# Kernel tuning notes

Measured on AMD Instinct MI355X. Metric: run time of the kernel, lower is better.

Reference implementation:

```python
import jax, jax.numpy as jnp
import numpy as np

B, C, W, H = 8, 256, 64, 64
DQK = C // 8  # 32


def setup_inputs() -> dict:
    key = jax.random.key(0)
    ks = jax.random.split(key, 5)
    x = jax.random.normal(ks[0], (B, C, W, H), dtype=jnp.float32)
    # 1x1 conv weights as [out_ch, in_ch]; scaled ~ spectral-normalized magnitude
    w_q = jax.random.normal(ks[1], (DQK, C), dtype=jnp.float32) * (1.0 / np.sqrt(C))
    w_k = jax.random.normal(ks[2], (DQK, C), dtype=jnp.float32) * (1.0 / np.sqrt(C))
    w_v = jax.random.normal(ks[3], (C, C), dtype=jnp.float32) * (1.0 / np.sqrt(C))
    b_q = jnp.zeros((DQK,), dtype=jnp.float32)
    b_k = jnp.zeros((DQK,), dtype=jnp.float32)
    b_v = jnp.zeros((C,), dtype=jnp.float32)
    gamma = jax.random.normal(ks[4], (1,), dtype=jnp.float32)
    return {"x": x, "w_q": w_q, "b_q": b_q, "w_k": w_k, "b_k": b_k,
            "w_v": w_v, "b_v": b_v, "gamma": gamma}


def reference(x, w_q, b_q, w_k, b_k, w_v, b_v, gamma):
    b, c, w, h = x.shape
    n = w * h
    xf = x.reshape(b, c, n)  # [B, C, N]
    # 1x1 convs == channel-mixing matmuls
    q = jnp.einsum('dc,bcn->bnd', w_q, xf) + b_q  # [B, N, Dqk]
    k = jnp.einsum('dc,bcn->bdn', w_k, xf) + b_k[None, :, None]  # [B, Dqk, N]
    v = jnp.einsum('oc,bcn->bon', w_v, xf) + b_v[None, :, None]  # [B, C, N]
    energy = jnp.einsum('bnd,bdm->bnm', q, k)  # [B, N, N]
    attn = jax.nn.softmax(energy, axis=-1)
    # out[b,c,i] = sum_j v[b,c,j] * attn[b,i,j]  (bmm(v, attn^T))
    out = jnp.einsum('bcj,bij->bci', v, attn).reshape(b, c, w, h)
    return gamma[0] * out + x
```

## Files before the change

kernel.cpp:

```cpp
#include <hip/hip_runtime.h>
#include <hip/hip_bf16.h>

typedef __attribute__((ext_vector_type(8))) short short8;
typedef __attribute__((ext_vector_type(4))) float f32x4;
typedef __attribute__((ext_vector_type(16))) float f32x16;

#define NB 8
#define NC 256
#define NN 4096
#define ND 32
#define NCH 16
#define LOG2E 1.44269504088896340736f

#define PIDX(row, col) (((row) << 8) + ((col) ^ (((row) & 15) << 3)))

static __device__ __forceinline__ ushort f2bf(float f) {
  __hip_bfloat16 h = __float2bfloat16(f);
  return reinterpret_cast<ushort&>(h);
}

__global__ __launch_bounds__(256, 4)
void proj_kernel(const float* __restrict__ x,
                 const float* __restrict__ wq, const float* __restrict__ bq,
                 const float* __restrict__ wk, const float* __restrict__ bk,
                 const float* __restrict__ wv, const float* __restrict__ bv,
                 ushort* __restrict__ qk, ushort* __restrict__ vt) {
  __shared__ float Xs[16][128];
  __shared__ float Ws[16][64];
  const int n0 = blockIdx.x * 128;
  const int o0 = blockIdx.y * 64;
  const int b  = blockIdx.z;
  const int t  = threadIdx.x;
  const int og4 = t & 15;
  const int ng  = t >> 4;

  float acc[4][8];
#pragma unroll
  for (int i = 0; i < 4; ++i)
#pragma unroll
    for (int j = 0; j < 8; ++j) acc[i][j] = 0.f;

  const int xs_r = t >> 4;
  const int xs_c = (t & 15) * 4;
  const int ws_o = t & 63;
  const int ws_c = (t >> 6) * 4;
  const float* wrow;
  {
    const int o = o0 + ws_o;
    if (o < 32)      wrow = wq + (size_t)o * NC;
    else if (o < 64) wrow = wk + (size_t)(o - 32) * NC;
    else             wrow = wv + (size_t)(o - 64) * NC;
  }

  for (int c0 = 0; c0 < NC; c0 += 16) {
    __syncthreads();
    const float* xsrc = x + ((size_t)(b * NC + c0 + xs_r)) * NN + n0;
    *(float4*)&Xs[xs_r][xs_c]      = *(const float4*)(xsrc + xs_c);
    *(float4*)&Xs[xs_r][64 + xs_c] = *(const float4*)(xsrc + 64 + xs_c);
    {
      const float4 wv4 = *(const float4*)(wrow + c0 + ws_c);
      Ws[ws_c + 0][ws_o] = wv4.x;
      Ws[ws_c + 1][ws_o] = wv4.y;
      Ws[ws_c + 2][ws_o] = wv4.z;
      Ws[ws_c + 3][ws_o] = wv4.w;
    }
    __syncthreads();
#pragma unroll
    for (int cc = 0; cc < 16; ++cc) {
      const float4 wv4 = *(const float4*)&Ws[cc][og4 * 4];
      const float4 xa  = *(const float4*)&Xs[cc][ng * 8];
      const float4 xb  = *(const float4*)&Xs[cc][ng * 8 + 4];
      const float wvv[4] = {wv4.x, wv4.y, wv4.z, wv4.w};
      const float xaa[8] = {xa.x, xa.y, xa.z, xa.w, xb.x, xb.y, xb.z, xb.w};
#pragma unroll
      for (int i = 0; i < 4; ++i)
#pragma unroll
        for (int j = 0; j < 8; ++j) acc[i][j] += wvv[i] * xaa[j];
    }
  }

  if (blockIdx.y == 0) {
    float bb[4], sc[4];
#pragma unroll
    for (int i = 0; i < 4; ++i) {
      const int o = og4 * 4 + i;
      bb[i] = (o < 32) ? bq[o] : bk[o - 32];
      sc[i] = (o < 32) ? LOG2E : 1.0f;
    }
#pragma unroll
    for (int j = 0; j < 8; ++j) {
      union { ushort u[4]; uint2 v; } pk;
#pragma unroll
      for (int i = 0; i < 4; ++i) pk.u[i] = f2bf((acc[i][j] + bb[i]) * sc[i]);
      *(uint2*)(qk + ((size_t)(b * NN + n0 + ng * 8 + j)) * 64 + og4 * 4) = pk.v;
    }
  } else {
#pragma unroll
    for (int i = 0; i < 4; ++i) {
      const int c = o0 - 64 + og4 * 4 + i;
      const float bb = bv[c];
      union { ushort u[8]; uint4 v; } pk;
#pragma unroll
      for (int j = 0; j < 8; ++j) pk.u[j] = f2bf(acc[i][j] + bb);
      *(uint4*)(vt + ((size_t)(b * NC + c)) * NN + n0 + ng * 8) = pk.v;
    }
  }
}

__global__ __launch_bounds__(512, 1)
void attn_kernel(const ushort* __restrict__ qk, const ushort* __restrict__ vt,
                 const float* __restrict__ x, const float* __restrict__ gamma,
                 float* __restrict__ out) {
  __shared__ __align__(16) ushort P[2][128 * 256];
  __shared__ __align__(16) float lL[128];

  const int lin  = blockIdx.x;
  const int b    = lin & 7;
  const int i0   = (lin >> 3) * 128;
  const int t    = threadIdx.x;
  const int w    = t >> 6;
  const int lane = t & 63;
  const int g16  = lane >> 4;
  const int c16  = lane & 15;
  const int l5   = lane >> 5;
  const int c32  = lane & 31;

  const f32x4 zero = {0.f, 0.f, 0.f, 0.f};
  const bool isS = (w < 4);

  const int prow0 = w * 32 + c16;
  const int prow1 = prow0 + 16;
  short8 qf0, qf1;
  short8 kf[8];
  float lp0 = 0.f, lp1 = 0.f;
  const ushort* kbase = qk + ((size_t)b * NN) * 64 + 32 + g16 * 8;
  if (isS) {
    qf0 = *(const short8*)(qk + ((size_t)(b * NN + i0 + prow0)) * 64 + g16 * 8);
    qf1 = *(const short8*)(qk + ((size_t)(b * NN + i0 + prow1)) * 64 + g16 * 8);
  }

  const int p = w - 4;
  f32x16 OA[4], OB[4];
  const ushort* vbA = nullptr; const ushort* vbB = nullptr;
  if (!isS) {
#pragma unroll
    for (int isub = 0; isub < 4; ++isub)
#pragma unroll
      for (int e = 0; e < 16; ++e) { OA[isub][e] = 0.f; OB[isub][e] = 0.f; }
    vbA = vt + ((size_t)(b * NC + p * 64 + c32)) * NN + l5 * 8;
    vbB = vt + ((size_t)(b * NC + p * 64 + 32 + c32)) * NN + l5 * 8;
  }

  for (int iv = 0; iv <= NCH; ++iv) {
    if (isS) {
      if (iv < NCH) {
        ushort* Pb = P[iv & 1];
        const ushort* kch = kbase + (size_t)iv * 256 * 64;
#pragma unroll
        for (int h = 0; h < 2; ++h) {
#pragma unroll
          for (int jt = 0; jt < 8; ++jt)
            kf[jt] = *(const short8*)(
                kch + (size_t)(h * 128 + jt * 16 + c16) * 64);
#pragma unroll
          for (int jt = 0; jt < 8; ++jt) {
            const f32x4 s0 = __builtin_amdgcn_mfma_f32_16x16x32_bf16(
                kf[jt], qf0, zero, 0, 0, 0);
            const f32x4 s1 = __builtin_amdgcn_mfma_f32_16x16x32_bf16(
                kf[jt], qf1, zero, 0, 0, 0);
            union { ushort u[4]; uint2 v; } pk0, pk1;
#pragma unroll
            for (int r = 0; r < 4; ++r) {
              const float e0 = exp2f(s0[r]);
              const float e1 = exp2f(s1[r]);
              lp0 += e0; lp1 += e1;
              pk0.u[r] = f2bf(e0); pk1.u[r] = f2bf(e1);
            }
            const int col = h * 128 + jt * 16 + g16 * 4;
            *(uint2*)&Pb[PIDX(prow0, col)] = pk0.v;
            *(uint2*)&Pb[PIDX(prow1, col)] = pk1.v;
          }
        }
      } else {
        lp0 += __shfl_xor(lp0, 16); lp0 += __shfl_xor(lp0, 32);
        lp1 += __shfl_xor(lp1, 16); lp1 += __shfl_xor(lp1, 32);
        if (g16 == 0) { lL[prow0] = lp0; lL[prow1] = lp1; }
      }
    } else if (iv >= 1) {
      const int ch = iv - 1;
      const ushort* Pb = P[ch & 1];
      const int j0 = ch * 256;
      __builtin_amdgcn_s_setprio(1);
#pragma unroll
      for (int ji = 0; ji < 16; ++ji) {
        const int jo = ji * 16;
        const short8 vf0 = *(const short8*)(vbA + j0 + jo);
        const short8 vf1 = *(const short8*)(vbB + j0 + jo);
#pragma unroll
        for (int isub = 0; isub < 4; ++isub) {
          const short8 pa =
              *(const short8*)&Pb[PIDX(isub * 32 + c32, jo + l5 * 8)];
          OA[isub] = __builtin_amdgcn_mfma_f32_32x32x16_bf16(
              pa, vf0, OA[isub], 0, 0, 0);
          OB[isub] = __builtin_amdgcn_mfma_f32_32x32x16_bf16(
              pa, vf1, OB[isub], 0, 0, 0);
        }
      }
      __builtin_amdgcn_s_setprio(0);
    }
    __syncthreads();
  }

  if (!isS) {
    const float g = gamma[0];
#pragma unroll
    for (int isub = 0; isub < 4; ++isub) {
#pragma unroll
      for (int q = 0; q < 4; ++q) {
        const int r0 = isub * 32 + q * 8 + l5 * 4;
        const f32x4 li = *(const f32x4*)&lL[r0];
        f32x4 gi;
#pragma unroll
        for (int r = 0; r < 4; ++r) gi[r] = g / li[r];
        {
          const int c = p * 64 + c32;
          const size_t base = ((size_t)(b * NC + c)) * NN + i0 + r0;
          const f32x4 xv = *(const f32x4*)(x + base);
          f32x4 ov;
#pragma unroll
          for (int r = 0; r < 4; ++r) ov[r] = OA[isub][q * 4 + r] * gi[r] + xv[r];
          *(f32x4*)(out + base) = ov;
        }
        {
          const int c = p * 64 + 32 + c32;
          const size_t base = ((size_t)(b * NC + c)) * NN + i0 + r0;
          const f32x4 xv = *(const f32x4*)(x + base);
          f32x4 ov;
#pragma unroll
          for (int r = 0; r < 4; ++r) ov[r] = OB[isub][q * 4 + r] * gi[r] + xv[r];
          *(f32x4*)(out + base) = ov;
        }
      }
    }
  }
}

extern "C" void kernel_launch(void* const* d_in, const int* in_sizes, int n_in,
                              void* d_out, int out_size, void* d_ws, size_t ws_size,
                              hipStream_t stream) {
  const float* x  = (const float*)d_in[0];
  const float* wq = (const float*)d_in[1];
  const float* bq = (const float*)d_in[2];
  const float* wk = (const float*)d_in[3];
  const float* bk = (const float*)d_in[4];
  const float* wv = (const float*)d_in[5];
  const float* bv = (const float*)d_in[6];
  const float* gm = (const float*)d_in[7];
  float* outp = (float*)d_out;

  ushort* qkw = (ushort*)d_ws;
  ushort* vtw = qkw + (size_t)NB * NN * 64;

  proj_kernel<<<dim3(NN / 128, 5, NB), 256, 0, stream>>>(
      x, wq, bq, wk, bk, wv, bv, qkw, vtw);
  attn_kernel<<<dim3((NN / 128) * NB), 512, 0, stream>>>(qkw, vtw, x, gm, outp);
}
```

Baseline: 180.7 us.

## Split attention work across 16 waves per block and prefetch V fragments

Doubles the attention block to 1024 threads: 8 score waves each own 16 query rows instead of 32, and 8 PV waves each own 32 channels instead of 64. This halves per-wave accumulator and register state, which should allow more concurrent waves and more latency hiding. It also double-buffers the V fragment global loads one step ahead. The tradeoff is that each K and P fragment load is now amortized over fewer MFMAs, so LDS and L2 traffic per MFMA rises. The launch_bounds(1024,4) hint also cannot be met with 128KB of LDS per block.

```diff
diff --git a/kernel.cpp b/kernel.cpp
--- a/kernel.cpp
+++ b/kernel.cpp
@@ -107,7 +107,7 @@
   }
 }
 
-__global__ __launch_bounds__(512, 1)
+__global__ __launch_bounds__(1024, 4)
 void attn_kernel(const ushort* __restrict__ qk, const ushort* __restrict__ vt,
                  const float* __restrict__ x, const float* __restrict__ gamma,
                  float* __restrict__ out) {
@@ -126,29 +126,26 @@
   const int c32  = lane & 31;
 
   const f32x4 zero = {0.f, 0.f, 0.f, 0.f};
-  const bool isS = (w < 4);
-
-  const int prow0 = w * 32 + c16;
-  const int prow1 = prow0 + 16;
-  short8 qf0, qf1;
+  const bool isS = (w < 8);
+
+  const int prow = w * 16 + c16;
+  short8 qf;
   short8 kf[8];
-  float lp0 = 0.f, lp1 = 0.f;
+  float lp = 0.f;
   const ushort* kbase = qk + ((size_t)b * NN) * 64 + 32 + g16 * 8;
   if (isS) {
-    qf0 = *(const short8*)(qk + ((size_t)(b * NN + i0 + prow0)) * 64 + g16 * 8);
-    qf1 = *(const short8*)(qk + ((size_t)(b * NN + i0 + prow1)) * 64 + g16 * 8);
-  }
-
-  const int p = w - 4;
-  f32x16 OA[4], OB[4];
-  const ushort* vbA = nullptr; const ushort* vbB = nullptr;
+    qf = *(const short8*)(qk + ((size_t)(b * NN + i0 + prow)) * 64 + g16 * 8);
+  }
+
+  const int p = w - 8;
+  f32x16 OA[4];
+  const ushort* vbA = nullptr;
   if (!isS) {
 #pragma unroll
     for (int isub = 0; isub < 4; ++isub)
 #pragma unroll
-      for (int e = 0; e < 16; ++e) { OA[isub][e] = 0.f; OB[isub][e] = 0.f; }
-    vbA = vt + ((size_t)(b * NC + p * 64 + c32)) * NN + l5 * 8;
-    vbB = vt + ((size_t)(b * NC + p * 64 + 32 + c32)) * NN + l5 * 8;
+      for (int e = 0; e < 16; ++e) OA[isub][e] = 0.f;
+    vbA = vt + ((size_t)(b * NC + p * 32 + c32)) * NN + l5 * 8;
   }
 
   for (int iv = 0; iv <= NCH; ++iv) {
@@ -165,45 +162,40 @@
 #pragma unroll
           for (int jt = 0; jt < 8; ++jt) {
             const f32x4 s0 = __builtin_amdgcn_mfma_f32_16x16x32_bf16(
-                kf[jt], qf0, zero, 0, 0, 0);
-            const f32x4 s1 = __builtin_amdgcn_mfma_f32_16x16x32_bf16(
-                kf[jt], qf1, zero, 0, 0, 0);
-            union { ushort u[4]; uint2 v; } pk0, pk1;
+                kf[jt], qf, zero, 0, 0, 0);
+            union { ushort u[4]; uint2 v; } pk;
 #pragma unroll
             for (int r = 0; r < 4; ++r) {
               const float e0 = exp2f(s0[r]);
-              const float e1 = exp2f(s1[r]);
-              lp0 += e0; lp1 += e1;
-              pk0.u[r] = f2bf(e0); pk1.u[r] = f2bf(e1);
+              lp += e0;
+              pk.u[r] = f2bf(e0);
             }
-            const int col = h * 128 + jt * 16 + g16 * 4;
-            *(uint2*)&Pb[PIDX(prow0, col)] = pk0.v;
-            *(uint2*)&Pb[PIDX(prow1, col)] = pk1.v;
+            *(uint2*)&Pb[PIDX(prow, h * 128 + jt * 16 + g16 * 4)] = pk.v;
           }
         }
       } else {
-        lp0 += __shfl_xor(lp0, 16); lp0 += __shfl_xor(lp0, 32);
-        lp1 += __shfl_xor(lp1, 16); lp1 += __shfl_xor(lp1, 32);
-        if (g16 == 0) { lL[prow0] = lp0; lL[prow1] = lp1; }
+        lp += __shfl_xor(lp, 16); lp += __shfl_xor(lp, 32);
+        if (g16 == 0) lL[prow] = lp;
       }
     } else if (iv >= 1) {
       const int ch = iv - 1;
       const ushort* Pb = P[ch & 1];
       const int j0 = ch * 256;
+      short8 vf[2];
+      vf[0] = *(const short8*)(vbA + j0);
       __builtin_amdgcn_s_setprio(1);
 #pragma unroll
       for (int ji = 0; ji < 16; ++ji) {
+        if (ji + 1 < 16)
+          vf[(ji + 1) & 1] = *(const short8*)(vbA + j0 + (ji + 1) * 16);
         const int jo = ji * 16;
-        const short8 vf0 = *(const short8*)(vbA + j0 + jo);
-        const short8 vf1 = *(const short8*)(vbB + j0 + jo);
+        const short8 v0 = vf[ji & 1];
 #pragma unroll
         for (int isub = 0; isub < 4; ++isub) {
           const short8 pa =
               *(const short8*)&Pb[PIDX(isub * 32 + c32, jo + l5 * 8)];
           OA[isub] = __builtin_amdgcn_mfma_f32_32x32x16_bf16(
-              pa, vf0, OA[isub], 0, 0, 0);
-          OB[isub] = __builtin_amdgcn_mfma_f32_32x32x16_bf16(
-              pa, vf1, OB[isub], 0, 0, 0);
+              pa, v0, OA[isub], 0, 0, 0);
         }
       }
       __builtin_amdgcn_s_setprio(0);
@@ -222,24 +214,13 @@
         f32x4 gi;
 #pragma unroll
         for (int r = 0; r < 4; ++r) gi[r] = g / li[r];
-        {
-          const int c = p * 64 + c32;
-          const size_t base = ((size_t)(b * NC + c)) * NN + i0 + r0;
-          const f32x4 xv = *(const f32x4*)(x + base);
-          f32x4 ov;
-#pragma unroll
-          for (int r = 0; r < 4; ++r) ov[r] = OA[isub][q * 4 + r] * gi[r] + xv[r];
-          *(f32x4*)(out + base) = ov;
-        }
-        {
-          const int c = p * 64 + 32 + c32;
-          const size_t base = ((size_t)(b * NC + c)) * NN + i0 + r0;
-          const f32x4 xv = *(const f32x4*)(x + base);
-          f32x4 ov;
-#pragma unroll
-          for (int r = 0; r < 4; ++r) ov[r] = OB[isub][q * 4 + r] * gi[r] + xv[r];
-          *(f32x4*)(out + base) = ov;
-        }
+        const int c = p * 32 + c32;
+        const size_t base = ((size_t)(b * NC + c)) * NN + i0 + r0;
+        const f32x4 xv = *(const f32x4*)(x + base);
+        f32x4 ov;
+#pragma unroll
+        for (int r = 0; r < 4; ++r) ov[r] = OA[isub][q * 4 + r] * gi[r] + xv[r];
+        *(f32x4*)(out + base) = ov;
       }
     }
   }
@@ -263,5 +244,5 @@
 
   proj_kernel<<<dim3(NN / 128, 5, NB), 256, 0, stream>>>(
       x, wq, bq, wk, bk, wv, bv, qkw, vtw);
-  attn_kernel<<<dim3((NN / 128) * NB), 512, 0, stream>>>(qkw, vtw, x, gm, outp);
-}
+  attn_kernel<<<dim3((NN / 128) * NB), 1024, 0, stream>>>(qkw, vtw, x, gm, outp);
+}
```

Result: slower. 235.2 us (+30.2%).

## Double-buffer K fragments across chunks and software-pipeline V loads in PV

Applied to the files above, without the earlier changes.

The S-producing warps now prefetch the next chunk's 16 K fragments into a second register set while computing the current chunk, with the loop unrolled by two to ping-pong the kfA/kfB sets. The PV warps load V fragments one 32-column group ahead of the MFMAs that consume them. The intent is to hide global-load latency behind MFMA and exp work in both roles. In exchange, register pressure rises sharply (32 short8 for K) under a 512-thread, single-block launch bound, which risks spills.

```diff
diff --git a/kernel.cpp b/kernel.cpp
--- a/kernel.cpp
+++ b/kernel.cpp
@@ -107,6 +107,79 @@
   }
 }
 
+#define S_BODY(IV, KCUR, KNXT)                                                \
+  do {                                                                        \
+    ushort* Pb = P[(IV) & 1];                                                 \
+    if ((IV) + 1 < NCH) {                                                     \
+      const ushort* kn = kbase + (size_t)((IV) + 1) * 256 * 64;               \
+      _Pragma("unroll")                                                       \
+      for (int jt = 0; jt < 16; ++jt)                                         \
+        KNXT[jt] = *(const short8*)(kn + (size_t)(jt * 16 + c16) * 64);       \
+    }                                                                         \
+    _Pragma("unroll")                                                         \
+    for (int jt = 0; jt < 16; ++jt) {                                         \
+      const f32x4 s0 = __builtin_amdgcn_mfma_f32_16x16x32_bf16(               \
+          KCUR[jt], qf0, zero, 0, 0, 0);                                      \
+      const f32x4 s1 = __builtin_amdgcn_mfma_f32_16x16x32_bf16(               \
+          KCUR[jt], qf1, zero, 0, 0, 0);                                      \
+      union { ushort u[4]; uint2 v; } pk0, pk1;                               \
+      _Pragma("unroll")                                                       \
+      for (int r = 0; r < 4; ++r) {                                           \
+        const float e0 = exp2f(s0[r]);                                        \
+        const float e1 = exp2f(s1[r]);                                        \
+        lp0 += e0; lp1 += e1;                                                 \
+        pk0.u[r] = f2bf(e0); pk1.u[r] = f2bf(e1);                             \
+      }                                                                       \
+      const int col = jt * 16 + g16 * 4;                                      \
+      *(uint2*)&Pb[PIDX(prow0, col)] = pk0.v;                                 \
+      *(uint2*)&Pb[PIDX(prow1, col)] = pk1.v;                                 \
+    }                                                                         \
+  } while (0)
+
+#define PV_LOADG(VSET, J0, G)                                                 \
+  do {                                                                        \
+    VSET[0] = *(const short8*)(vbA + (J0) + (G) * 32);                        \
+    VSET[1] = *(const short8*)(vbB + (J0) + (G) * 32);                        \
+    VSET[2] = *(const short8*)(vbA + (J0) + (G) * 32 + 16);                   \
+    VSET[3] = *(const short8*)(vbB + (J0) + (G) * 32 + 16);                   \
+  } while (0)
+
+#define PV_COMPG(VSET, Pb, J0, G)                                             \
+  do {                                                                        \
+    _Pragma("unroll")                                                         \
+    for (int k = 0; k < 2; ++k) {                                             \
+      const int jo = (G) * 32 + k * 16;                                       \
+      _Pragma("unroll")                                                       \
+      for (int isub = 0; isub < 4; ++isub) {                                  \
+        const short8 pa =                                                     \
+            *(const short8*)&Pb[PIDX(isub * 32 + c32, jo + l5 * 8)];          \
+        OA[isub] = __builtin_amdgcn_mfma_f32_32x32x16_bf16(                   \
+            pa, VSET[k * 2], OA[isub], 0, 0, 0);                              \
+        OB[isub] = __builtin_amdgcn_mfma_f32_32x32x16_bf16(                   \
+            pa, VSET[k * 2 + 1], OB[isub], 0, 0, 0);                          \
+      }                                                                       \
+    }                                                                         \
+  } while (0)
+
+#define PV_BODY(IV)                                                           \
+  do {                                                                        \
+    const int ch = (IV) - 1;                                                  \
+    const ushort* Pb = P[ch & 1];                                             \
+    const int j0 = ch * 256;                                                  \
+    short8 vA[4], vB[4];                                                      \
+    PV_LOADG(vA, j0, 0);                                                      \
+    __builtin_amdgcn_s_setprio(1);                                            \
+    PV_LOADG(vB, j0, 1);  PV_COMPG(vA, Pb, j0, 0);                            \
+    PV_LOADG(vA, j0, 2);  PV_COMPG(vB, Pb, j0, 1);                            \
+    PV_LOADG(vB, j0, 3);  PV_COMPG(vA, Pb, j0, 2);                            \
+    PV_LOADG(vA, j0, 4);  PV_COMPG(vB, Pb, j0, 3);                            \
+    PV_LOADG(vB, j0, 5);  PV_COMPG(vA, Pb, j0, 4);                            \
+    PV_LOADG(vA, j0, 6);  PV_COMPG(vB, Pb, j0, 5);                            \
+    PV_LOADG(vB, j0, 7);  PV_COMPG(vA, Pb, j0, 6);                            \
+    PV_COMPG(vB, Pb, j0, 7);                                                  \
+    __builtin_amdgcn_s_setprio(0);                                            \
+  } while (0)
+
 __global__ __launch_bounds__(512, 1)
 void attn_kernel(const ushort* __restrict__ qk, const ushort* __restrict__ vt,
                  const float* __restrict__ x, const float* __restrict__ gamma,
@@ -131,12 +204,15 @@
   const int prow0 = w * 32 + c16;
   const int prow1 = prow0 + 16;
   short8 qf0, qf1;
-  short8 kf[8];
+  short8 kfA[16], kfB[16];
   float lp0 = 0.f, lp1 = 0.f;
   const ushort* kbase = qk + ((size_t)b * NN) * 64 + 32 + g16 * 8;
   if (isS) {
     qf0 = *(const short8*)(qk + ((size_t)(b * NN + i0 + prow0)) * 64 + g16 * 8);
     qf1 = *(const short8*)(qk + ((size_t)(b * NN + i0 + prow1)) * 64 + g16 * 8);
+#pragma unroll
+    for (int jt = 0; jt < 16; ++jt)
+      kfA[jt] = *(const short8*)(kbase + (size_t)(jt * 16 + c16) * 64);
   }
 
   const int p = w - 4;
@@ -151,65 +227,22 @@
     vbB = vt + ((size_t)(b * NC + p * 64 + 32 + c32)) * NN + l5 * 8;
   }
 
-  for (int iv = 0; iv <= NCH; ++iv) {
-    if (isS) {
-      if (iv < NCH) {
-        ushort* Pb = P[iv & 1];
-        const ushort* kch = kbase + (size_t)iv * 256 * 64;
-#pragma unroll
-        for (int h = 0; h < 2; ++h) {
-#pragma unroll
-          for (int jt = 0; jt < 8; ++jt)
-            kf[jt] = *(const short8*)(
-                kch + (size_t)(h * 128 + jt * 16 + c16) * 64);
-#pragma unroll
-          for (int jt = 0; jt < 8; ++jt) {
-            const f32x4 s0 = __builtin_amdgcn_mfma_f32_16x16x32_bf16(
-                kf[jt], qf0, zero, 0, 0, 0);
-            const f32x4 s1 = __builtin_amdgcn_mfma_f32_16x16x32_bf16(
-                kf[jt], qf1, zero, 0, 0, 0);
-            union { ushort u[4]; uint2 v; } pk0, pk1;
-#pragma unroll
-            for (int r = 0; r < 4; ++r) {
-              const float e0 = exp2f(s0[r]);
-              const float e1 = exp2f(s1[r]);
-              lp0 += e0; lp1 += e1;
-              pk0.u[r] = f2bf(e0); pk1.u[r] = f2bf(e1);
-            }
-            const int col = h * 128 + jt * 16 + g16 * 4;
-            *(uint2*)&Pb[PIDX(prow0, col)] = pk0.v;
-            *(uint2*)&Pb[PIDX(prow1, col)] = pk1.v;
-          }
-        }
-      } else {
-        lp0 += __shfl_xor(lp0, 16); lp0 += __shfl_xor(lp0, 32);
-        lp1 += __shfl_xor(lp1, 16); lp1 += __shfl_xor(lp1, 32);
-        if (g16 == 0) { lL[prow0] = lp0; lL[prow1] = lp1; }
-      }
-    } else if (iv >= 1) {
-      const int ch = iv - 1;
-      const ushort* Pb = P[ch & 1];
-      const int j0 = ch * 256;
-      __builtin_amdgcn_s_setprio(1);
-#pragma unroll
-      for (int ji = 0; ji < 16; ++ji) {
-        const int jo = ji * 16;
-        const short8 vf0 = *(const short8*)(vbA + j0 + jo);
-        const short8 vf1 = *(const short8*)(vbB + j0 + jo);
-#pragma unroll
-        for (int isub = 0; isub < 4; ++isub) {
-          const short8 pa =
-              *(const short8*)&Pb[PIDX(isub * 32 + c32, jo + l5 * 8)];
-          OA[isub] = __builtin_amdgcn_mfma_f32_32x32x16_bf16(
-              pa, vf0, OA[isub], 0, 0, 0);
-          OB[isub] = __builtin_amdgcn_mfma_f32_32x32x16_bf16(
-              pa, vf1, OB[isub], 0, 0, 0);
-        }
-      }
-      __builtin_amdgcn_s_setprio(0);
-    }
+  for (int iv2 = 0; iv2 < NCH; iv2 += 2) {
+    if (isS) S_BODY(iv2, kfA, kfB);
+    else if (iv2 >= 1) PV_BODY(iv2);
     __syncthreads();
-  }
+    if (isS) S_BODY(iv2 + 1, kfB, kfA);
+    else PV_BODY(iv2 + 1);
+    __syncthreads();
+  }
+  if (isS) {
+    lp0 += __shfl_xor(lp0, 16); lp0 += __shfl_xor(lp0, 32);
+    lp1 += __shfl_xor(lp1, 16); lp1 += __shfl_xor(lp1, 32);
+    if (g16 == 0) { lL[prow0] = lp0; lL[prow1] = lp1; }
+  } else {
+    PV_BODY(NCH);
+  }
+  __syncthreads();
 
   if (!isS) {
     const float g = gamma[0];
```

Result: slower. 341.0 us (+88.7%).

## Rewrite projection kernel with bf16 MFMA using split hi/lo weights

Applied to the files above, without the earlier changes.

Replaces the scalar FP32 FMA projection GEMM with bf16 MFMA 16x16x32 instructions. Weights are split into a bf16 high part and a bf16 residual so the weight side keeps extra precision, while x is rounded to bf16. The whole weight tile is staged once in LDS, and the V output is transposed through LDS to get coalesced 16-byte stores. This cuts ALU time in the projection stage at the cost of more LDS use, lower occupancy (launch bounds 2), and bf16 rounding of the input activations.

```diff
diff --git a/kernel.cpp b/kernel.cpp
--- a/kernel.cpp
+++ b/kernel.cpp
@@ -18,92 +18,131 @@
   __hip_bfloat16 h = __float2bfloat16(f);
   return reinterpret_cast<ushort&>(h);
 }
-
-__global__ __launch_bounds__(256, 4)
+static __device__ __forceinline__ float bf2f(ushort u) {
+  const uint v = ((uint)u) << 16;
+  return __builtin_bit_cast(float, v);
+}
+
+#define LDW 264
+#define LDX 40
+#define LDO 136
+
+__global__ __launch_bounds__(256, 2)
 void proj_kernel(const float* __restrict__ x,
                  const float* __restrict__ wq, const float* __restrict__ bq,
                  const float* __restrict__ wk, const float* __restrict__ bk,
                  const float* __restrict__ wv, const float* __restrict__ bv,
                  ushort* __restrict__ qk, ushort* __restrict__ vt) {
-  __shared__ float Xs[16][128];
-  __shared__ float Ws[16][64];
+  __shared__ __align__(16) ushort Ws[2][64 * LDW];
+  __shared__ __align__(16) ushort Xs[128 * LDX];
+
   const int n0 = blockIdx.x * 128;
   const int o0 = blockIdx.y * 64;
   const int b  = blockIdx.z;
   const int t  = threadIdx.x;
-  const int og4 = t & 15;
-  const int ng  = t >> 4;
-
-  float acc[4][8];
-#pragma unroll
-  for (int i = 0; i < 4; ++i)
-#pragma unroll
-    for (int j = 0; j < 8; ++j) acc[i][j] = 0.f;
-
-  const int xs_r = t >> 4;
-  const int xs_c = (t & 15) * 4;
-  const int ws_o = t & 63;
-  const int ws_c = (t >> 6) * 4;
-  const float* wrow;
+  const int w  = t >> 6;
+  const int lane = t & 63;
+  const int g16  = lane >> 4;
+  const int c16  = lane & 15;
+
   {
-    const int o = o0 + ws_o;
-    if (o < 32)      wrow = wq + (size_t)o * NC;
-    else if (o < 64) wrow = wk + (size_t)(o - 32) * NC;
-    else             wrow = wv + (size_t)(o - 64) * NC;
-  }
-
-  for (int c0 = 0; c0 < NC; c0 += 16) {
-    __syncthreads();
-    const float* xsrc = x + ((size_t)(b * NC + c0 + xs_r)) * NN + n0;
-    *(float4*)&Xs[xs_r][xs_c]      = *(const float4*)(xsrc + xs_c);
-    *(float4*)&Xs[xs_r][64 + xs_c] = *(const float4*)(xsrc + 64 + xs_c);
+    const int o  = t >> 2;
+    const int cb = (t & 3) * 64;
+    const int oa = o0 + o;
+    const float* wrow;
+    float scale = 1.0f;
+    if (oa < 32)       { wrow = wq + (size_t)oa * NC; scale = LOG2E; }
+    else if (oa < 64)  { wrow = wk + (size_t)(oa - 32) * NC; }
+    else               { wrow = wv + (size_t)(oa - 64) * NC; }
+#pragma unroll
+    for (int cc = 0; cc < 64; cc += 8) {
+      const float4 f0 = *(const float4*)(wrow + cb + cc);
+      const float4 f1 = *(const float4*)(wrow + cb + cc + 4);
+      float v[8] = {f0.x, f0.y, f0.z, f0.w, f1.x, f1.y, f1.z, f1.w};
+      union { ushort u[8]; uint4 q; } hi, lo;
+#pragma unroll
+      for (int e = 0; e < 8; ++e) {
+        const float s = v[e] * scale;
+        const ushort h = f2bf(s);
+        hi.u[e] = h;
+        lo.u[e] = f2bf(s - bf2f(h));
+      }
+      *(uint4*)&Ws[0][o * LDW + cb + cc] = hi.q;
+      *(uint4*)&Ws[1][o * LDW + cb + cc] = lo.q;
+    }
+  }
+
+  f32x4 acc[8];
+#pragma unroll
+  for (int nt = 0; nt < 8; ++nt)
+#pragma unroll
+    for (int r = 0; r < 4; ++r) acc[nt][r] = 0.f;
+
+  const int s_cc = w * 8 + (lane >> 3);
+  const int s_nb = (lane & 7) * 4;
+
+  for (int c0 = 0; c0 < NC; c0 += 32) {
+    __syncthreads();
     {
-      const float4 wv4 = *(const float4*)(wrow + c0 + ws_c);
-      Ws[ws_c + 0][ws_o] = wv4.x;
-      Ws[ws_c + 1][ws_o] = wv4.y;
-      Ws[ws_c + 2][ws_o] = wv4.z;
-      Ws[ws_c + 3][ws_o] = wv4.w;
-    }
-    __syncthreads();
-#pragma unroll
-    for (int cc = 0; cc < 16; ++cc) {
-      const float4 wv4 = *(const float4*)&Ws[cc][og4 * 4];
-      const float4 xa  = *(const float4*)&Xs[cc][ng * 8];
-      const float4 xb  = *(const float4*)&Xs[cc][ng * 8 + 4];
-      const float wvv[4] = {wv4.x, wv4.y, wv4.z, wv4.w};
-      const float xaa[8] = {xa.x, xa.y, xa.z, xa.w, xb.x, xb.y, xb.z, xb.w};
-#pragma unroll
-      for (int i = 0; i < 4; ++i)
-#pragma unroll
-        for (int j = 0; j < 8; ++j) acc[i][j] += wvv[i] * xaa[j];
+      const float* xsrc = x + ((size_t)(b * NC + c0 + s_cc)) * NN + n0 + s_nb;
+#pragma unroll
+      for (int it = 0; it < 4; ++it) {
+        const float4 f = *(const float4*)(xsrc + it * 32);
+        const int n = s_nb + it * 32;
+        Xs[(n + 0) * LDX + s_cc] = f2bf(f.x);
+        Xs[(n + 1) * LDX + s_cc] = f2bf(f.y);
+        Xs[(n + 2) * LDX + s_cc] = f2bf(f.z);
+        Xs[(n + 3) * LDX + s_cc] = f2bf(f.w);
+      }
+    }
+    __syncthreads();
+
+    const short8 ah = *(const short8*)&Ws[0][(w * 16 + c16) * LDW + c0 + g16 * 8];
+    const short8 al = *(const short8*)&Ws[1][(w * 16 + c16) * LDW + c0 + g16 * 8];
+#pragma unroll
+    for (int nt = 0; nt < 8; ++nt) {
+      const short8 bf = *(const short8*)&Xs[(nt * 16 + c16) * LDX + g16 * 8];
+      acc[nt] = __builtin_amdgcn_mfma_f32_16x16x32_bf16(ah, bf, acc[nt], 0, 0, 0);
+      acc[nt] = __builtin_amdgcn_mfma_f32_16x16x32_bf16(al, bf, acc[nt], 0, 0, 0);
     }
   }
 
   if (blockIdx.y == 0) {
-    float bb[4], sc[4];
-#pragma unroll
-    for (int i = 0; i < 4; ++i) {
-      const int o = og4 * 4 + i;
-      bb[i] = (o < 32) ? bq[o] : bk[o - 32];
-      sc[i] = (o < 32) ? LOG2E : 1.0f;
-    }
-#pragma unroll
-    for (int j = 0; j < 8; ++j) {
+    float bb[4];
+#pragma unroll
+    for (int r = 0; r < 4; ++r) {
+      const int o = w * 16 + g16 * 4 + r;
+      bb[r] = (o < 32) ? bq[o] * LOG2E : bk[o - 32];
+    }
+#pragma unroll
+    for (int nt = 0; nt < 8; ++nt) {
       union { ushort u[4]; uint2 v; } pk;
 #pragma unroll
-      for (int i = 0; i < 4; ++i) pk.u[i] = f2bf((acc[i][j] + bb[i]) * sc[i]);
-      *(uint2*)(qk + ((size_t)(b * NN + n0 + ng * 8 + j)) * 64 + og4 * 4) = pk.v;
+      for (int r = 0; r < 4; ++r) pk.u[r] = f2bf(acc[nt][r] + bb[r]);
+      const int n = n0 + nt * 16 + c16;
+      *(uint2*)(qk + ((size_t)(b * NN + n)) * 64 + w * 16 + g16 * 4) = pk.v;
     }
   } else {
-#pragma unroll
-    for (int i = 0; i < 4; ++i) {
-      const int c = o0 - 64 + og4 * 4 + i;
-      const float bb = bv[c];
-      union { ushort u[8]; uint4 v; } pk;
-#pragma unroll
-      for (int j = 0; j < 8; ++j) pk.u[j] = f2bf(acc[i][j] + bb);
-      *(uint4*)(vt + ((size_t)(b * NC + c)) * NN + n0 + ng * 8) = pk.v;
-    }
+    const int ch0 = o0 - 64;
+    float bb[4];
+#pragma unroll
+    for (int r = 0; r < 4; ++r) bb[r] = bv[ch0 + w * 16 + g16 * 4 + r];
+    __syncthreads();
+    ushort* Os = &Ws[0][0];
+#pragma unroll
+    for (int nt = 0; nt < 8; ++nt) {
+#pragma unroll
+      for (int r = 0; r < 4; ++r)
+        Os[(w * 16 + g16 * 4 + r) * LDO + nt * 16 + c16] =
+            f2bf(acc[nt][r] + bb[r]);
+    }
+    __syncthreads();
+    const int chl = t >> 2;
+    const int nb  = (t & 3) * 32;
+    ushort* dst = vt + ((size_t)(b * NC + ch0 + chl)) * NN + n0 + nb;
+#pragma unroll
+    for (int k = 0; k < 4; ++k)
+      *(uint4*)(dst + k * 8) = *(const uint4*)&Os[chl * LDO + nb + k * 8];
   }
 }
 
```

Result: faster. 150.6 us (-16.7%).
